# Kernel tuning notes

Measured on AMD Instinct MI355X. Metric: run time of the kernel, lower is better.

Reference implementation:

```python
import jax, jax.numpy as jnp
import numpy as np
import math

NUM_SEGS = 16  # label ids in gt are in [0, NUM_SEGS); 0 = background
NP_RATIO = 3
PI = np.float32(math.pi)


def cart2polar(coord):
    # coord: (N, 2, H, W) -> normalized polar angle in [0, 1)
    x = coord[:, 0]
    y = coord[:, 1]
    theta = jnp.arctan(y / (x + np.float32(1e-12)))
    theta = theta + (x < 0).astype(coord.dtype) * PI
    theta = theta + ((x > 0) & (y < 0)).astype(coord.dtype) * (2 * PI)
    return theta / (2 * PI)


def cal_weight(gt2d):
    # gt2d: (H, W) int labels. Per-segment average weight:
    # each pixel of segment s>0 gets (posCount / nSegPresent) / count(s).
    flat = gt2d.reshape(-1)
    counts = jnp.zeros((NUM_SEGS,), jnp.float32).at[flat].add(1.0)
    pos_counts = counts.at[0].set(0.0)  # labels = unique(gt)[1:] drops background 0
    pos_count = pos_counts.sum()
    nseg = (pos_counts > 0).sum().astype(jnp.float32)
    seg_ave = pos_count / jnp.maximum(nseg, 1.0)
    pix = seg_ave / jnp.maximum(counts, 1.0)  # per-label pixel weight
    return jnp.where(gt2d > 0, pix[gt2d], np.float32(0.0))


def setup_inputs() -> dict:
    key = jax.random.key(0)
    k1, k2, k3 = jax.random.split(key, 3)
    N, C, H, W = 8, 2, 1024, 1024
    pred = jax.random.normal(k1, (N, C, H, W), dtype=jnp.float32)
    gt_df = jax.random.normal(k2, (N, C, H, W), dtype=jnp.float32)
    gt = jax.random.randint(k3, (N, 1, H, W), 0, NUM_SEGS, dtype=jnp.int32)
    return {"pred": pred, "gt_df": gt_df, "gt": gt}


def reference(pred, gt_df, gt):
    N, _, H, W = pred.shape
    dist = pred - gt_df
    distL2 = dist * dist
    angle = cart2polar(gt_df) - cart2polar(pred)          # (N,H,W)
    term = distL2[:, 0] + distL2[:, 1] + angle * angle    # (N,H,W)

    weight = jax.vmap(lambda g: cal_weight(g[0]))(gt)     # (N,H,W) positive-region weights
    regionNeg = (weight == 0).astype(jnp.float32)
    sumPos = (weight > 0).astype(jnp.float32).sum(axis=(1, 2))
    sumNeg = regionNeg.sum(axis=(1, 2))
    k = jnp.minimum(NP_RATIO * sumPos, sumNeg).astype(jnp.int32)  # hard negatives per sample

    # OHEM: keep the k largest negative-region losses per sample
    lossFlat = (term * regionNeg).reshape(N, H * W)
    order = jnp.argsort(lossFlat, axis=1)
    rank = jnp.argsort(order, axis=1)  # rank of each element in ascending order
    keep = rank >= (H * W - k[:, None])
    mask = (keep & (lossFlat != 0)).astype(jnp.float32).reshape(N, H, W)  # weightNeg indicator

    # Faithful to torch broadcast: weightPos (N,H,W) + weightNeg (N,1,H,W) -> (N,N,H,W),
    # computed here without materializing the (N,N,H,W) tensor:
    # sum_{i,j,hw} term[j]*(weight[j] + mask[i]) = N*sum(term*weight) + sum_hw(term.sum(0)*mask.sum(0))
    num = N * jnp.sum(term * weight) + jnp.sum(term.sum(axis=0) * mask.sum(axis=0))
    denom = N * (weight.sum() + mask.sum())
    return num / N / 2.0 / denom
```

## Files before the change

kernel.cpp:

```cpp
#include <hip/hip_runtime.h>
#include <math.h>

#define NBATCH 8
#define HWN (1024*1024)
#define NGRP (HWN/4)
#define MAINB 1024


static __device__ __forceinline__ float polar01(float x, float y) {
    float r = y * __builtin_amdgcn_rcpf(x + 1e-12f);
    float ar = fabsf(r);
    float inv = __builtin_amdgcn_rcpf(ar);
    bool big = ar > 1.0f;
    float t = big ? inv : ar;
    float s = t * t;
    float p = -0.0117212f;
    p = fmaf(p, s,  0.05265332f);
    p = fmaf(p, s, -0.11643287f);
    p = fmaf(p, s,  0.19354346f);
    p = fmaf(p, s, -0.33262348f);
    p = fmaf(p, s,  0.99997726f);
    float a = t * p;
    a = big ? (1.57079632679489662f - a) : a;
    a = copysignf(a, r);
    if (x < 0.f) a += 3.14159274101257324f;
    else if (x > 0.f && y < 0.f) a += 6.28318548202514648f;
    return a * 0.15915494309189535f;
}

static __device__ __forceinline__ void block_reduce2(double& a, double& b) {
    for (int o = 32; o; o >>= 1) { a += __shfl_down(a, o); b += __shfl_down(b, o); }
    __shared__ double sa[4], sb[4];
    int w = threadIdx.x >> 6, l = threadIdx.x & 63;
    if (l == 0) { sa[w] = a; sb[w] = b; }
    __syncthreads();
    if (threadIdx.x == 0) { a = sa[0]+sa[1]+sa[2]+sa[3]; b = sb[0]+sb[1]+sb[2]+sb[3]; }
    __syncthreads();
}

static __device__ __forceinline__ void block_reduce3(double& a, double& b, double& c) {
    for (int o = 32; o; o >>= 1) { a += __shfl_down(a, o); b += __shfl_down(b, o); c += __shfl_down(c, o); }
    __shared__ double sa[4], sb[4], sc[4];
    int w = threadIdx.x >> 6, l = threadIdx.x & 63;
    if (l == 0) { sa[w] = a; sb[w] = b; sc[w] = c; }
    __syncthreads();
    if (threadIdx.x == 0) {
        a = sa[0]+sa[1]+sa[2]+sa[3]; b = sb[0]+sb[1]+sb[2]+sb[3]; c = sc[0]+sc[1]+sc[2]+sc[3];
    }
    __syncthreads();
}

__global__ __launch_bounds__(256) void k_hist(const int* __restrict__ gt,
        unsigned* __restrict__ countsRep) {
    int tid = threadIdx.x;
    int n = blockIdx.x >> 8;
    int jb = blockIdx.x & 255;
    const int4* g4 = (const int4*)(gt + (size_t)n * HWN);
    unsigned c[16];
#pragma unroll
    for (int b = 0; b < 16; ++b) c[b] = 0u;
#pragma unroll
    for (int k = 0; k < 4; ++k) {
        int4 g = g4[jb * 1024 + k * 256 + tid];
#pragma unroll
        for (int e = 0; e < 4; ++e) {
            int gv = (&g.x)[e] & 15;
#pragma unroll
            for (int b = 0; b < 16; ++b) c[b] += (unsigned)__popcll(__ballot(gv == b));
        }
    }
    if ((tid & 63) == 0) {
        int copy = (blockIdx.x * 4 + (tid >> 6)) & 31;
        unsigned* dst = countsRep + copy * 128 + n * 16;
#pragma unroll
        for (int b = 0; b < 16; ++b) atomicAdd(&dst[b], c[b]);
    }
}

__global__ void k_stats(const unsigned* __restrict__ countsRep, float* __restrict__ pix,
                        int* __restrict__ kv, int* __restrict__ mode,
                        double* __restrict__ g_wsum, unsigned* __restrict__ anySlow) {
    int tid = threadIdx.x;
    __shared__ unsigned sc[128];
    __shared__ int smd[NBATCH];
    __shared__ double sws[NBATCH];
    if (tid < 128) {
        unsigned s = 0;
        for (int c = 0; c < 32; ++c) s += countsRep[c * 128 + tid];
        sc[tid] = s;
    }
    __syncthreads();
    if (tid < NBATCH) {
        int n = tid;
        long long sumPos = 0; int nseg = 0;
        for (int s = 1; s < 16; ++s) { sumPos += sc[n*16+s]; nseg += sc[n*16+s] ? 1 : 0; }
        long long sumNeg = sc[n*16];
        float seg_ave = (float)sumPos / (float)(nseg ? nseg : 1);
        double ws = 0.0;
        pix[n*16] = 0.f;
        for (int s = 1; s < 16; ++s) {
            unsigned cc = sc[n*16+s];
            float pv = seg_ave / (float)(cc > 1u ? cc : 1u);
            pix[n*16+s] = pv;
            ws += (double)pv * (double)cc;
        }
        long long k = 3 * sumPos; if (sumNeg < k) k = sumNeg;
        kv[n] = (int)k;
        int md = (k <= 0) ? 0 : ((k >= sumNeg) ? 1 : 2);
        mode[n] = md; smd[n] = md; sws[n] = ws;
    }
    __syncthreads();
    if (tid == 0) {
        double w = 0.0; unsigned as = 0u;
        for (int i = 0; i < NBATCH; ++i) { w += sws[i]; as |= (smd[i] == 2) ? 1u : 0u; }
        *g_wsum = w; *anySlow = as;
    }
}

__global__ __launch_bounds__(256) void k_main(const float* __restrict__ pred,
        const float* __restrict__ gdf, const int* __restrict__ gt,
        const float* __restrict__ pix, const int* __restrict__ mode,
        float* __restrict__ lossBuf, unsigned short* __restrict__ tsumBuf,
        unsigned* __restrict__ h1G, double* __restrict__ pN1,
        double* __restrict__ pS2, double* __restrict__ pC) {
    __shared__ float spix[128];
    __shared__ int smode[NBATCH];
    __shared__ unsigned h1[NBATCH * 256];
    int tid = threadIdx.x;
    if (tid < 128) spix[tid] = pix[tid];
    if (tid < NBATCH) smode[tid] = mode[tid];
    for (int i = tid; i < NBATCH * 256; i += 256) h1[i] = 0u;
    __syncthreads();

    int j = blockIdx.x * 256 + tid;
    float tsum[4] = {0.f, 0.f, 0.f, 0.f};
    int   cntE[4] = {0, 0, 0, 0};
    float num1f = 0.f;
#pragma unroll 2
    for (int n = 0; n < NBATCH; ++n) {
        float4 px4 = ((const float4*)(pred + ((size_t)(2 * n)    ) * HWN))[j];
        float4 py4 = ((const float4*)(pred + ((size_t)(2 * n) + 1) * HWN))[j];
        float4 gx4 = ((const float4*)(gdf  + ((size_t)(2 * n)    ) * HWN))[j];
        float4 gy4 = ((const float4*)(gdf  + ((size_t)(2 * n) + 1) * HWN))[j];
        int4   g4  = ((const int4*)  (gt   + (size_t)n * HWN))[j];
        int m = smode[n];
        float4 lossv;
#pragma unroll
        for (int e = 0; e < 4; ++e) {
            float px = (&px4.x)[e], py = (&py4.x)[e];
            float gx = (&gx4.x)[e], gy = (&gy4.x)[e];
            int   g  = (&g4.x)[e] & 15;
            float dx = px - gx, dy = py - gy;
            float ang = polar01(gx, gy) - polar01(px, py);
            float t = dx * dx + dy * dy + ang * ang;
            tsum[e] += t;
            num1f += t * spix[n * 16 + g];
            if (m == 1) {
                if (g == 0 && t != 0.f) cntE[e]++;
            } else if (m == 2) {
                float lv = (g == 0) ? t : 0.f;
                (&lossv.x)[e] = lv;
                unsigned u = __float_as_uint(lv);
                if (u) atomicAdd(&h1[n * 256 + (u >> 24)], 1u);
            }
        }
        if (m == 2) ((float4*)(lossBuf + (size_t)n * HWN))[j] = lossv;
    }
    ushort4 tz;
#pragma unroll
    for (int e = 0; e < 4; ++e) {
        unsigned u = __float_as_uint(tsum[e]);
        (&tz.x)[e] = (unsigned short)((u + 0x7FFFu + ((u >> 16) & 1u)) >> 16);
    }
    ((ushort4*)tsumBuf)[j] = tz;

    float spec2 = 0.f, cntS = 0.f;
#pragma unroll
    for (int e = 0; e < 4; ++e) { spec2 += tsum[e] * (float)cntE[e]; cntS += (float)cntE[e]; }

    double a = (double)num1f, b = (double)spec2, c = (double)cntS;
    block_reduce3(a, b, c);
    if (tid == 0) { pN1[blockIdx.x] = a; pS2[blockIdx.x] = b; pC[blockIdx.x] = c; }

    __syncthreads();
    int copy = blockIdx.x & 7;
    for (int i = tid; i < NBATCH * 256; i += 256) {
        unsigned v = h1[i];
        if (v) atomicAdd(&h1G[copy * 2048 + i], v);
    }
}

__global__ void k_scanA(const unsigned* __restrict__ h1G, const int* __restrict__ kv,
        const int* __restrict__ mode, unsigned* __restrict__ stMode,
        unsigned* __restrict__ stPfx, unsigned* __restrict__ stK,
        unsigned* __restrict__ stT, unsigned* __restrict__ active,
        const double* __restrict__ pN1, const double* __restrict__ pS2,
        const double* __restrict__ pC, double* __restrict__ g_num1,
        double* __restrict__ g_acc, double* __restrict__ g_cnt) {
    int tid = threadIdx.x;
    double a = 0, b = 0, c = 0;
    for (int i = tid; i < MAINB; i += 256) { a += pN1[i]; b += pS2[i]; c += pC[i]; }
    block_reduce3(a, b, c);
    if (tid == 0) { *g_num1 = a; *g_acc = b; *g_cnt = c; }
    __shared__ unsigned h[256];
    __shared__ unsigned rw[4];
    for (int n = 0; n < NBATCH; ++n) {
        if (mode[n] != 2) continue;
        unsigned s = 0;
        for (int c8 = 0; c8 < 8; ++c8) s += h1G[c8 * 2048 + n * 256 + tid];
        h[tid] = s;
        unsigned v = s;
        for (int o = 32; o; o >>= 1) v += __shfl_down(v, o);
        int w = tid >> 6, l = tid & 63;
        if (l == 0) rw[w] = v;
        __syncthreads();
        if (tid == 0) {
            unsigned nnz = rw[0] + rw[1] + rw[2] + rw[3];
            unsigned k = (unsigned)kv[n];
            if (k >= nnz) { stT[n] = 0u; stMode[n] = 0u; }
            else {
                unsigned cum = 0; int b1 = 0;
                for (int bb = 255; bb >= 0; --bb) { if (cum + h[bb] >= k) { b1 = bb; break; } cum += h[bb]; }
                stMode[n] = 1u; stPfx[n] = (unsigned)b1; stK[n] = k - cum; active[1] = 1u;
            }
        }
        __syncthreads();
    }
}

__global__ __launch_bounds__(256) void k_refine(const float* __restrict__ lossBuf,
        const unsigned* __restrict__ stMode, const unsigned* __restrict__ stPfx,
        unsigned* __restrict__ hist, int level, const unsigned* __restrict__ active) {
    if (active[level] == 0u) return;
    unsigned md[NBATCH], pf[NBATCH];
#pragma unroll
    for (int n = 0; n < NBATCH; ++n) { md[n] = stMode[n]; pf[n] = stPfx[n]; }
    int ms = 32 - 8 * level, hs = 24 - 8 * level;
    int stride = gridDim.x * blockDim.x;
    for (int j = blockIdx.x * blockDim.x + threadIdx.x; j < NGRP; j += stride) {
#pragma unroll
        for (int n = 0; n < NBATCH; ++n) {
            if (md[n] != (unsigned)level) continue;
            float4 lv = ((const float4*)(lossBuf + (size_t)n * HWN))[j];
#pragma unroll
            for (int e = 0; e < 4; ++e) {
                unsigned u = __float_as_uint((&lv.x)[e]);
                if (u != 0u && (u >> ms) == pf[n])
                    atomicAdd(&hist[n * 256 + ((u >> hs) & 255u)], 1u);
            }
        }
    }
}

__global__ void k_scanN(unsigned* __restrict__ stMode, unsigned* __restrict__ stPfx,
        unsigned* __restrict__ stK, unsigned* __restrict__ stT,
        const unsigned* __restrict__ hist, int level, unsigned* __restrict__ active) {
    if (active[level] == 0u) return;
    int n = blockIdx.x;
    if (stMode[n] != (unsigned)level) return;
    __shared__ unsigned h[256];
    h[threadIdx.x] = hist[n * 256 + threadIdx.x];
    __syncthreads();
    if (threadIdx.x == 0) {
        unsigned k2 = stK[n], cum = 0; int bb = 0;
        for (int b = 255; b >= 0; --b) { if (cum + h[b] >= k2) { bb = b; break; } cum += h[b]; }
        unsigned np = (stPfx[n] << 8) | (unsigned)bb;
        stK[n] = k2 - cum;
        if (level == 3) { stT[n] = np; stMode[n] = 0u; }
        else            { stPfx[n] = np; stMode[n] = (unsigned)(level + 1); active[level + 1] = 1u; }
    }
}

__global__ __launch_bounds__(256) void k_num2(const float* __restrict__ lossBuf,
        const unsigned short* __restrict__ tsumBuf, const unsigned* __restrict__ stT,
        const int* __restrict__ mode, const unsigned* __restrict__ anySlow,
        double* __restrict__ g_acc, double* __restrict__ g_cnt) {
    if (*anySlow == 0u) return;
    int j = blockIdx.x * 256 + threadIdx.x;
    ushort4 tz = ((const ushort4*)tsumBuf)[j];
    float ts[4];
#pragma unroll
    for (int e = 0; e < 4; ++e) ts[e] = __uint_as_float(((unsigned)(&tz.x)[e]) << 16);
    double acc = 0.0, cnt = 0.0;
#pragma unroll
    for (int n = 0; n < NBATCH; ++n) {
        if (mode[n] != 2) continue;
        unsigned T = stT[n];
        float4 lv = ((const float4*)(lossBuf + (size_t)n * HWN))[j];
#pragma unroll
        for (int e = 0; e < 4; ++e) {
            unsigned u = __float_as_uint((&lv.x)[e]);
            if (u != 0u && u >= T) { acc += (double)ts[e]; cnt += 1.0; }
        }
    }
    block_reduce2(acc, cnt);
    if (threadIdx.x == 0) { atomicAdd(g_acc, acc); atomicAdd(g_cnt, cnt); }
}

__global__ void k_result(const double* __restrict__ g_num1, const double* __restrict__ g_wsum,
        const double* __restrict__ g_acc, const double* __restrict__ g_cnt,
        float* __restrict__ out) {
    double num = (double)NBATCH * g_num1[0] + g_acc[0];
    double den = (double)NBATCH * (g_wsum[0] + g_cnt[0]);
    out[0] = (float)(num / (double)NBATCH / 2.0 / den);
}


extern "C" void kernel_launch(void* const* d_in, const int* in_sizes, int n_in,
                              void* d_out, int out_size, void* d_ws, size_t ws_size,
                              hipStream_t stream) {
    const float* pred = (const float*)d_in[0];
    const float* gdf  = (const float*)d_in[1];
    const int*   gt   = (const int*)d_in[2];
    float* out = (float*)d_out;

    char* W = (char*)d_ws;
    float* lossBuf = (float*)W;
    unsigned short* tsumBuf = (unsigned short*)(W + 33554432);
    char* Z = W + 35651584;
    unsigned* countsRep = (unsigned*)Z;
    unsigned* h1G    = (unsigned*)(Z + 16384);
    unsigned* hA     = (unsigned*)(Z + 81920);
    unsigned* hB     = (unsigned*)(Z + 90112);
    unsigned* hC     = (unsigned*)(Z + 98304);
    unsigned* stMode = (unsigned*)(Z + 106496);
    unsigned* stPfx  = (unsigned*)(Z + 106528);
    unsigned* stK    = (unsigned*)(Z + 106560);
    unsigned* stT    = (unsigned*)(Z + 106592);
    unsigned* active = (unsigned*)(Z + 106624);
    unsigned* anySlow= (unsigned*)(Z + 106640);
    double*   g_num1 = (double*)(Z + 106648);
    double*   g_wsum = (double*)(Z + 106656);
    double*   g_acc  = (double*)(Z + 106664);
    double*   g_cnt  = (double*)(Z + 106672);
    const size_t ZBYTES = 106680;
    char* P = Z + ZBYTES;
    float* pix  = (float*)P;
    int*   kv   = (int*)(P + 512);
    int*   mode = (int*)(P + 544);
    double* pN1 = (double*)(P + 576);
    double* pS2 = (double*)(P + 8768);
    double* pC  = (double*)(P + 16960);

    size_t need = 35651584 + ZBYTES + 25152;
    if (ws_size < need) return;

    hipMemsetAsync(Z, 0, ZBYTES, stream);
    k_hist  <<<2048, 256, 0, stream>>>(gt, countsRep);
    k_stats <<<1, 256, 0, stream>>>(countsRep, pix, kv, mode, g_wsum, anySlow);
    k_main  <<<MAINB, 256, 0, stream>>>(pred, gdf, gt, pix, mode, lossBuf, tsumBuf,
                                        h1G, pN1, pS2, pC);
    k_scanA <<<1, 256, 0, stream>>>(h1G, kv, mode, stMode, stPfx, stK, stT, active,
                                    pN1, pS2, pC, g_num1, g_acc, g_cnt);
    k_refine<<<1024, 256, 0, stream>>>(lossBuf, stMode, stPfx, hA, 1, active);
    k_scanN <<<NBATCH, 256, 0, stream>>>(stMode, stPfx, stK, stT, hA, 1, active);
    k_refine<<<1024, 256, 0, stream>>>(lossBuf, stMode, stPfx, hB, 2, active);
    k_scanN <<<NBATCH, 256, 0, stream>>>(stMode, stPfx, stK, stT, hB, 2, active);
    k_refine<<<1024, 256, 0, stream>>>(lossBuf, stMode, stPfx, hC, 3, active);
    k_scanN <<<NBATCH, 256, 0, stream>>>(stMode, stPfx, stK, stT, hC, 3, active);
    k_num2  <<<MAINB, 256, 0, stream>>>(lossBuf, tsumBuf, stT, mode, anySlow, g_acc, g_cnt);
    k_result<<<1, 1, 0, stream>>>(g_num1, g_wsum, g_acc, g_cnt, out);
}
```

Measured before the change: 223.1 us.

## Collapse the OHEM pipeline into three kernels with a 16-bit radix histogram

Replaces the memset, stats, scan, three refine, three scan-step, num2 and result launches with three kernels. `k_hist` writes per-block label counts in a transposed layout and zeroes a 64K-bin histogram. `k_main` recomputes per-sample statistics in every block, uses float2 loads, and writes the bf16 tsum buffer only when some sample needs top-k selection. A single-block `k_tail` does the final reductions and a two-level threshold search over the 16-bit histogram. This removes launch and serialization overhead and a 2 MB write in the common case. The price is global atomics on a large histogram and a single-block slow path for the top-k case.

```diff
diff --git a/kernel.cpp b/kernel.cpp
--- a/kernel.cpp
+++ b/kernel.cpp
@@ -3,8 +3,9 @@
 
 #define NBATCH 8
 #define HWN (1024*1024)
-#define NGRP (HWN/4)
-#define MAINB 1024
+#define NPAIR (HWN/2)
+#define HB 512
+#define MB 2048
 
 
 static __device__ __forceinline__ float polar01(float x, float y) {
@@ -40,55 +41,157 @@
 
 static __device__ __forceinline__ void block_reduce3(double& a, double& b, double& c) {
     for (int o = 32; o; o >>= 1) { a += __shfl_down(a, o); b += __shfl_down(b, o); c += __shfl_down(c, o); }
-    __shared__ double sa[4], sb[4], sc[4];
+    __shared__ double sa[4], sb[4], sc4[4];
     int w = threadIdx.x >> 6, l = threadIdx.x & 63;
-    if (l == 0) { sa[w] = a; sb[w] = b; sc[w] = c; }
+    if (l == 0) { sa[w] = a; sb[w] = b; sc4[w] = c; }
     __syncthreads();
     if (threadIdx.x == 0) {
-        a = sa[0]+sa[1]+sa[2]+sa[3]; b = sb[0]+sb[1]+sb[2]+sb[3]; c = sc[0]+sc[1]+sc[2]+sc[3];
-    }
-    __syncthreads();
+        a = sa[0]+sa[1]+sa[2]+sa[3]; b = sb[0]+sb[1]+sb[2]+sb[3]; c = sc4[0]+sc4[1]+sc4[2]+sc4[3];
+    }
+    __syncthreads();
+}
+
+static __device__ __forceinline__ void load_counts(const unsigned* __restrict__ hcntT,
+                                                   unsigned* sc) {
+    int tid = threadIdx.x;
+    if (tid < 128) {
+        int n = tid >> 4, bin = tid & 15;
+        const uint4* p = (const uint4*)&hcntT[bin * HB + n * 64];
+        unsigned s = 0;
+#pragma unroll
+        for (int k = 0; k < 16; ++k) { uint4 v = p[k]; s += v.x + v.y + v.z + v.w; }
+        sc[tid] = s;
+    }
 }
 
 __global__ __launch_bounds__(256) void k_hist(const int* __restrict__ gt,
-        unsigned* __restrict__ countsRep) {
+        unsigned* __restrict__ hcntT, unsigned* __restrict__ h64) {
     int tid = threadIdx.x;
-    int n = blockIdx.x >> 8;
-    int jb = blockIdx.x & 255;
+    uint4 z; z.x = z.y = z.z = z.w = 0u;
+    ((uint4*)h64)[blockIdx.x * 256 + tid] = z;
+
+    int n = blockIdx.x >> 6, b = blockIdx.x & 63;
     const int4* g4 = (const int4*)(gt + (size_t)n * HWN);
     unsigned c[16];
 #pragma unroll
-    for (int b = 0; b < 16; ++b) c[b] = 0u;
-#pragma unroll
-    for (int k = 0; k < 4; ++k) {
-        int4 g = g4[jb * 1024 + k * 256 + tid];
+    for (int bin = 0; bin < 16; ++bin) c[bin] = 0u;
+#pragma unroll
+    for (int k = 0; k < 16; ++k) {
+        int4 g = g4[b * 4096 + k * 256 + tid];
 #pragma unroll
         for (int e = 0; e < 4; ++e) {
             int gv = (&g.x)[e] & 15;
 #pragma unroll
-            for (int b = 0; b < 16; ++b) c[b] += (unsigned)__popcll(__ballot(gv == b));
-        }
-    }
-    if ((tid & 63) == 0) {
-        int copy = (blockIdx.x * 4 + (tid >> 6)) & 31;
-        unsigned* dst = countsRep + copy * 128 + n * 16;
-#pragma unroll
-        for (int b = 0; b < 16; ++b) atomicAdd(&dst[b], c[b]);
-    }
-}
-
-__global__ void k_stats(const unsigned* __restrict__ countsRep, float* __restrict__ pix,
-                        int* __restrict__ kv, int* __restrict__ mode,
-                        double* __restrict__ g_wsum, unsigned* __restrict__ anySlow) {
+            for (int bin = 0; bin < 16; ++bin)
+                c[bin] += (unsigned)__popcll(__ballot(gv == bin));
+        }
+    }
+    __shared__ unsigned sw[4][16];
+    int wave = tid >> 6, lane = tid & 63;
+    if (lane == 0) {
+#pragma unroll
+        for (int bin = 0; bin < 16; ++bin) sw[wave][bin] = c[bin];
+    }
+    __syncthreads();
+    if (tid < 16) hcntT[tid * HB + blockIdx.x] = sw[0][tid] + sw[1][tid] + sw[2][tid] + sw[3][tid];
+}
+
+__global__ __launch_bounds__(256, 8) void k_main(const float* __restrict__ pred,
+        const float* __restrict__ gdf, const int* __restrict__ gt,
+        const unsigned* __restrict__ hcntT, float* __restrict__ lossBuf,
+        unsigned short* __restrict__ tsumBuf, unsigned* __restrict__ h64,
+        double* __restrict__ pN1, double* __restrict__ pS2, double* __restrict__ pC) {
+    __shared__ unsigned sc[128];
+    __shared__ float spix[128];
+    __shared__ int smode[NBATCH];
+    __shared__ int sAny;
     int tid = threadIdx.x;
+    load_counts(hcntT, sc);
+    if (tid == 0) sAny = 0;
+    __syncthreads();
+    if (tid < NBATCH) {
+        int n = tid;
+        long long sumPos = 0; int nseg = 0;
+        for (int s = 1; s < 16; ++s) { sumPos += sc[n*16+s]; nseg += sc[n*16+s] ? 1 : 0; }
+        long long sumNeg = sc[n*16];
+        float seg_ave = (float)sumPos / (float)(nseg ? nseg : 1);
+        spix[n*16] = 0.f;
+        for (int s = 1; s < 16; ++s) {
+            unsigned cc = sc[n*16+s];
+            spix[n*16+s] = seg_ave / (float)(cc > 1u ? cc : 1u);
+        }
+        long long k = 3 * sumPos; if (sumNeg < k) k = sumNeg;
+        int md = (k <= 0) ? 0 : ((k >= sumNeg) ? 1 : 2);
+        smode[n] = md;
+        if (md == 2) sAny = 1;
+    }
+    __syncthreads();
+    bool anySlow = (sAny != 0);
+
+    int j2 = blockIdx.x * 256 + tid;
+    float ts0 = 0.f, ts1 = 0.f, num1f = 0.f;
+    int c0 = 0, c1 = 0;
+#pragma unroll 2
+    for (int n = 0; n < NBATCH; ++n) {
+        float2 px2 = ((const float2*)(pred + ((size_t)(2*n)    ) * HWN))[j2];
+        float2 py2 = ((const float2*)(pred + ((size_t)(2*n) + 1) * HWN))[j2];
+        float2 gx2 = ((const float2*)(gdf  + ((size_t)(2*n)    ) * HWN))[j2];
+        float2 gy2 = ((const float2*)(gdf  + ((size_t)(2*n) + 1) * HWN))[j2];
+        int2   g2  = ((const int2*)  (gt   + (size_t)n * HWN))[j2];
+        int m = smode[n];
+        float dx0 = px2.x - gx2.x, dy0 = py2.x - gy2.x;
+        float a0 = polar01(gx2.x, gy2.x) - polar01(px2.x, py2.x);
+        float t0 = dx0*dx0 + dy0*dy0 + a0*a0;
+        float dx1 = px2.y - gx2.y, dy1 = py2.y - gy2.y;
+        float a1 = polar01(gx2.y, gy2.y) - polar01(px2.y, py2.y);
+        float t1 = dx1*dx1 + dy1*dy1 + a1*a1;
+        int gv0 = g2.x & 15, gv1 = g2.y & 15;
+        ts0 += t0; ts1 += t1;
+        num1f += t0 * spix[n*16 + gv0];
+        num1f += t1 * spix[n*16 + gv1];
+        if (m == 1) {
+            c0 += (gv0 == 0 && t0 != 0.f) ? 1 : 0;
+            c1 += (gv1 == 0 && t1 != 0.f) ? 1 : 0;
+        } else if (m == 2) {
+            float l0 = (gv0 == 0) ? t0 : 0.f;
+            float l1 = (gv1 == 0) ? t1 : 0.f;
+            float2 lv; lv.x = l0; lv.y = l1;
+            ((float2*)(lossBuf + (size_t)n * HWN))[j2] = lv;
+            unsigned u0 = __float_as_uint(l0), u1 = __float_as_uint(l1);
+            unsigned* hh = h64 + (size_t)(blockIdx.x & 7) * 65536;
+            if (u0) atomicAdd(&hh[u0 >> 16], 1u);
+            if (u1) atomicAdd(&hh[u1 >> 16], 1u);
+        }
+    }
+    if (anySlow) {
+        unsigned u0 = __float_as_uint(ts0), u1 = __float_as_uint(ts1);
+        ushort2 tz;
+        tz.x = (unsigned short)((u0 + 0x7FFFu + ((u0 >> 16) & 1u)) >> 16);
+        tz.y = (unsigned short)((u1 + 0x7FFFu + ((u1 >> 16) & 1u)) >> 16);
+        ((ushort2*)tsumBuf)[j2] = tz;
+    }
+    double a = (double)num1f;
+    double b = (double)(ts0 * (float)c0 + ts1 * (float)c1);
+    double c = (double)(c0 + c1);
+    block_reduce3(a, b, c);
+    if (tid == 0) { pN1[blockIdx.x] = a; pS2[blockIdx.x] = b; pC[blockIdx.x] = c; }
+}
+
+__global__ __launch_bounds__(256) void k_tail(const unsigned* __restrict__ hcntT,
+        const unsigned* __restrict__ h64, const float* __restrict__ lossBuf,
+        const unsigned short* __restrict__ tsumBuf, const double* __restrict__ pN1,
+        const double* __restrict__ pS2, const double* __restrict__ pC,
+        float* __restrict__ out) {
     __shared__ unsigned sc[128];
-    __shared__ int smd[NBATCH];
-    __shared__ double sws[NBATCH];
-    if (tid < 128) {
-        unsigned s = 0;
-        for (int c = 0; c < 32; ++c) s += countsRep[c * 128 + tid];
-        sc[tid] = s;
-    }
+    __shared__ double swsum[NBATCH];
+    __shared__ int smode[NBATCH];
+    __shared__ long long skv[NBATCH];
+    __shared__ unsigned part[256];
+    __shared__ unsigned fine[256];
+    __shared__ unsigned scoarse[2];
+    __shared__ double racc[2];
+    int tid = threadIdx.x;
+    load_counts(hcntT, sc);
     __syncthreads();
     if (tid < NBATCH) {
         int n = tid;
@@ -97,212 +200,94 @@
         long long sumNeg = sc[n*16];
         float seg_ave = (float)sumPos / (float)(nseg ? nseg : 1);
         double ws = 0.0;
-        pix[n*16] = 0.f;
         for (int s = 1; s < 16; ++s) {
             unsigned cc = sc[n*16+s];
             float pv = seg_ave / (float)(cc > 1u ? cc : 1u);
-            pix[n*16+s] = pv;
             ws += (double)pv * (double)cc;
         }
         long long k = 3 * sumPos; if (sumNeg < k) k = sumNeg;
-        kv[n] = (int)k;
-        int md = (k <= 0) ? 0 : ((k >= sumNeg) ? 1 : 2);
-        mode[n] = md; smd[n] = md; sws[n] = ws;
-    }
-    __syncthreads();
-    if (tid == 0) {
-        double w = 0.0; unsigned as = 0u;
-        for (int i = 0; i < NBATCH; ++i) { w += sws[i]; as |= (smd[i] == 2) ? 1u : 0u; }
-        *g_wsum = w; *anySlow = as;
-    }
-}
-
-__global__ __launch_bounds__(256) void k_main(const float* __restrict__ pred,
-        const float* __restrict__ gdf, const int* __restrict__ gt,
-        const float* __restrict__ pix, const int* __restrict__ mode,
-        float* __restrict__ lossBuf, unsigned short* __restrict__ tsumBuf,
-        unsigned* __restrict__ h1G, double* __restrict__ pN1,
-        double* __restrict__ pS2, double* __restrict__ pC) {
-    __shared__ float spix[128];
-    __shared__ int smode[NBATCH];
-    __shared__ unsigned h1[NBATCH * 256];
-    int tid = threadIdx.x;
-    if (tid < 128) spix[tid] = pix[tid];
-    if (tid < NBATCH) smode[tid] = mode[tid];
-    for (int i = tid; i < NBATCH * 256; i += 256) h1[i] = 0u;
-    __syncthreads();
-
-    int j = blockIdx.x * 256 + tid;
-    float tsum[4] = {0.f, 0.f, 0.f, 0.f};
-    int   cntE[4] = {0, 0, 0, 0};
-    float num1f = 0.f;
-#pragma unroll 2
+        skv[n] = k;
+        smode[n] = (k <= 0) ? 0 : ((k >= sumNeg) ? 1 : 2);
+        swsum[n] = ws;
+    }
+    __syncthreads();
+
+    double a = 0, b = 0, c = 0;
+    for (int i = tid; i < MB; i += 256) { a += pN1[i]; b += pS2[i]; c += pC[i]; }
+    block_reduce3(a, b, c);
+    if (tid == 0) { racc[0] = b; racc[1] = c; }
+    __syncthreads();
+
     for (int n = 0; n < NBATCH; ++n) {
-        float4 px4 = ((const float4*)(pred + ((size_t)(2 * n)    ) * HWN))[j];
-        float4 py4 = ((const float4*)(pred + ((size_t)(2 * n) + 1) * HWN))[j];
-        float4 gx4 = ((const float4*)(gdf  + ((size_t)(2 * n)    ) * HWN))[j];
-        float4 gy4 = ((const float4*)(gdf  + ((size_t)(2 * n) + 1) * HWN))[j];
-        int4   g4  = ((const int4*)  (gt   + (size_t)n * HWN))[j];
-        int m = smode[n];
-        float4 lossv;
-#pragma unroll
-        for (int e = 0; e < 4; ++e) {
-            float px = (&px4.x)[e], py = (&py4.x)[e];
-            float gx = (&gx4.x)[e], gy = (&gy4.x)[e];
-            int   g  = (&g4.x)[e] & 15;
-            float dx = px - gx, dy = py - gy;
-            float ang = polar01(gx, gy) - polar01(px, py);
-            float t = dx * dx + dy * dy + ang * ang;
-            tsum[e] += t;
-            num1f += t * spix[n * 16 + g];
-            if (m == 1) {
-                if (g == 0 && t != 0.f) cntE[e]++;
-            } else if (m == 2) {
-                float lv = (g == 0) ? t : 0.f;
-                (&lossv.x)[e] = lv;
-                unsigned u = __float_as_uint(lv);
-                if (u) atomicAdd(&h1[n * 256 + (u >> 24)], 1u);
-            }
-        }
-        if (m == 2) ((float4*)(lossBuf + (size_t)n * HWN))[j] = lossv;
-    }
-    ushort4 tz;
-#pragma unroll
-    for (int e = 0; e < 4; ++e) {
-        unsigned u = __float_as_uint(tsum[e]);
-        (&tz.x)[e] = (unsigned short)((u + 0x7FFFu + ((u >> 16) & 1u)) >> 16);
-    }
-    ((ushort4*)tsumBuf)[j] = tz;
-
-    float spec2 = 0.f, cntS = 0.f;
-#pragma unroll
-    for (int e = 0; e < 4; ++e) { spec2 += tsum[e] * (float)cntE[e]; cntS += (float)cntE[e]; }
-
-    double a = (double)num1f, b = (double)spec2, c = (double)cntS;
-    block_reduce3(a, b, c);
-    if (tid == 0) { pN1[blockIdx.x] = a; pS2[blockIdx.x] = b; pC[blockIdx.x] = c; }
-
-    __syncthreads();
-    int copy = blockIdx.x & 7;
-    for (int i = tid; i < NBATCH * 256; i += 256) {
-        unsigned v = h1[i];
-        if (v) atomicAdd(&h1G[copy * 2048 + i], v);
-    }
-}
-
-__global__ void k_scanA(const unsigned* __restrict__ h1G, const int* __restrict__ kv,
-        const int* __restrict__ mode, unsigned* __restrict__ stMode,
-        unsigned* __restrict__ stPfx, unsigned* __restrict__ stK,
-        unsigned* __restrict__ stT, unsigned* __restrict__ active,
-        const double* __restrict__ pN1, const double* __restrict__ pS2,
-        const double* __restrict__ pC, double* __restrict__ g_num1,
-        double* __restrict__ g_acc, double* __restrict__ g_cnt) {
-    int tid = threadIdx.x;
-    double a = 0, b = 0, c = 0;
-    for (int i = tid; i < MAINB; i += 256) { a += pN1[i]; b += pS2[i]; c += pC[i]; }
-    block_reduce3(a, b, c);
-    if (tid == 0) { *g_num1 = a; *g_acc = b; *g_cnt = c; }
-    __shared__ unsigned h[256];
-    __shared__ unsigned rw[4];
-    for (int n = 0; n < NBATCH; ++n) {
-        if (mode[n] != 2) continue;
-        unsigned s = 0;
-        for (int c8 = 0; c8 < 8; ++c8) s += h1G[c8 * 2048 + n * 256 + tid];
-        h[tid] = s;
-        unsigned v = s;
-        for (int o = 32; o; o >>= 1) v += __shfl_down(v, o);
-        int w = tid >> 6, l = tid & 63;
-        if (l == 0) rw[w] = v;
+        if (smode[n] != 2) continue;
+        unsigned loc = 0;
+        int base = tid * 256;
+        for (int i = 0; i < 256; ++i) {
+            unsigned s = 0;
+#pragma unroll
+            for (int r = 0; r < 8; ++r) s += h64[r * 65536 + base + i];
+            loc += s;
+        }
+        part[tid] = loc;
         __syncthreads();
         if (tid == 0) {
-            unsigned nnz = rw[0] + rw[1] + rw[2] + rw[3];
-            unsigned k = (unsigned)kv[n];
-            if (k >= nnz) { stT[n] = 0u; stMode[n] = 0u; }
+            long long nnz = 0;
+            for (int i = 0; i < 256; ++i) nnz += part[i];
+            long long k = skv[n];
+            if (k >= nnz) { scoarse[0] = 0xFFFFFFFFu; }
             else {
-                unsigned cum = 0; int b1 = 0;
-                for (int bb = 255; bb >= 0; --bb) { if (cum + h[bb] >= k) { b1 = bb; break; } cum += h[bb]; }
-                stMode[n] = 1u; stPfx[n] = (unsigned)b1; stK[n] = k - cum; active[1] = 1u;
+                unsigned cum = 0; int cc2 = 0;
+                for (int i = 255; i >= 0; --i) {
+                    if ((long long)cum + part[i] >= k) { cc2 = i; break; }
+                    cum += part[i];
+                }
+                scoarse[0] = (unsigned)cc2; scoarse[1] = cum;
             }
         }
         __syncthreads();
-    }
-}
-
-__global__ __launch_bounds__(256) void k_refine(const float* __restrict__ lossBuf,
-        const unsigned* __restrict__ stMode, const unsigned* __restrict__ stPfx,
-        unsigned* __restrict__ hist, int level, const unsigned* __restrict__ active) {
-    if (active[level] == 0u) return;
-    unsigned md[NBATCH], pf[NBATCH];
-#pragma unroll
-    for (int n = 0; n < NBATCH; ++n) { md[n] = stMode[n]; pf[n] = stPfx[n]; }
-    int ms = 32 - 8 * level, hs = 24 - 8 * level;
-    int stride = gridDim.x * blockDim.x;
-    for (int j = blockIdx.x * blockDim.x + threadIdx.x; j < NGRP; j += stride) {
-#pragma unroll
-        for (int n = 0; n < NBATCH; ++n) {
-            if (md[n] != (unsigned)level) continue;
-            float4 lv = ((const float4*)(lossBuf + (size_t)n * HWN))[j];
-#pragma unroll
-            for (int e = 0; e < 4; ++e) {
-                unsigned u = __float_as_uint((&lv.x)[e]);
-                if (u != 0u && (u >> ms) == pf[n])
-                    atomicAdd(&hist[n * 256 + ((u >> hs) & 255u)], 1u);
+        unsigned T = 0u;
+        if (scoarse[0] != 0xFFFFFFFFu) {
+            unsigned cc2 = scoarse[0];
+            unsigned s = 0;
+#pragma unroll
+            for (int r = 0; r < 8; ++r) s += h64[r * 65536 + cc2 * 256 + tid];
+            fine[tid] = s;
+            __syncthreads();
+            if (tid == 0) {
+                long long k = skv[n];
+                unsigned cum = scoarse[1]; int bb = 0;
+                for (int i = 255; i >= 0; --i) {
+                    if ((long long)cum + fine[i] >= k) { bb = i; break; }
+                    cum += fine[i];
+                }
+                scoarse[0] = (scoarse[0] << 8) | (unsigned)bb;
             }
-        }
-    }
-}
-
-__global__ void k_scanN(unsigned* __restrict__ stMode, unsigned* __restrict__ stPfx,
-        unsigned* __restrict__ stK, unsigned* __restrict__ stT,
-        const unsigned* __restrict__ hist, int level, unsigned* __restrict__ active) {
-    if (active[level] == 0u) return;
-    int n = blockIdx.x;
-    if (stMode[n] != (unsigned)level) return;
-    __shared__ unsigned h[256];
-    h[threadIdx.x] = hist[n * 256 + threadIdx.x];
-    __syncthreads();
-    if (threadIdx.x == 0) {
-        unsigned k2 = stK[n], cum = 0; int bb = 0;
-        for (int b = 255; b >= 0; --b) { if (cum + h[b] >= k2) { bb = b; break; } cum += h[b]; }
-        unsigned np = (stPfx[n] << 8) | (unsigned)bb;
-        stK[n] = k2 - cum;
-        if (level == 3) { stT[n] = np; stMode[n] = 0u; }
-        else            { stPfx[n] = np; stMode[n] = (unsigned)(level + 1); active[level + 1] = 1u; }
-    }
-}
-
-__global__ __launch_bounds__(256) void k_num2(const float* __restrict__ lossBuf,
-        const unsigned short* __restrict__ tsumBuf, const unsigned* __restrict__ stT,
-        const int* __restrict__ mode, const unsigned* __restrict__ anySlow,
-        double* __restrict__ g_acc, double* __restrict__ g_cnt) {
-    if (*anySlow == 0u) return;
-    int j = blockIdx.x * 256 + threadIdx.x;
-    ushort4 tz = ((const ushort4*)tsumBuf)[j];
-    float ts[4];
-#pragma unroll
-    for (int e = 0; e < 4; ++e) ts[e] = __uint_as_float(((unsigned)(&tz.x)[e]) << 16);
-    double acc = 0.0, cnt = 0.0;
-#pragma unroll
-    for (int n = 0; n < NBATCH; ++n) {
-        if (mode[n] != 2) continue;
-        unsigned T = stT[n];
-        float4 lv = ((const float4*)(lossBuf + (size_t)n * HWN))[j];
-#pragma unroll
-        for (int e = 0; e < 4; ++e) {
-            unsigned u = __float_as_uint((&lv.x)[e]);
-            if (u != 0u && u >= T) { acc += (double)ts[e]; cnt += 1.0; }
-        }
-    }
-    block_reduce2(acc, cnt);
-    if (threadIdx.x == 0) { atomicAdd(g_acc, acc); atomicAdd(g_cnt, cnt); }
-}
-
-__global__ void k_result(const double* __restrict__ g_num1, const double* __restrict__ g_wsum,
-        const double* __restrict__ g_acc, const double* __restrict__ g_cnt,
-        float* __restrict__ out) {
-    double num = (double)NBATCH * g_num1[0] + g_acc[0];
-    double den = (double)NBATCH * (g_wsum[0] + g_cnt[0]);
-    out[0] = (float)(num / (double)NBATCH / 2.0 / den);
+            __syncthreads();
+            T = scoarse[0] << 16;
+            __syncthreads();
+        }
+        double acc = 0.0, cnt = 0.0;
+        const float2* lp = (const float2*)(lossBuf + (size_t)n * HWN);
+        const ushort2* tp = (const ushort2*)tsumBuf;
+        for (int i = tid; i < NPAIR; i += 256) {
+            float2 lv = lp[i];
+            ushort2 tz = tp[i];
+            unsigned u0 = __float_as_uint(lv.x), u1 = __float_as_uint(lv.y);
+            if (u0 != 0u && u0 >= T) { acc += (double)__uint_as_float(((unsigned)tz.x) << 16); cnt += 1.0; }
+            if (u1 != 0u && u1 >= T) { acc += (double)__uint_as_float(((unsigned)tz.y) << 16); cnt += 1.0; }
+        }
+        block_reduce2(acc, cnt);
+        if (tid == 0) { racc[0] += acc; racc[1] += cnt; }
+        __syncthreads();
+    }
+
+    if (tid == 0) {
+        double wsum = 0.0;
+        for (int n = 0; n < NBATCH; ++n) wsum += swsum[n];
+        double num = (double)NBATCH * a + racc[0];
+        double den = (double)NBATCH * (wsum + racc[1]);
+        out[0] = (float)(num / (double)NBATCH / 2.0 / den);
+    }
 }
 
 
@@ -317,47 +302,16 @@
     char* W = (char*)d_ws;
     float* lossBuf = (float*)W;
     unsigned short* tsumBuf = (unsigned short*)(W + 33554432);
-    char* Z = W + 35651584;
-    unsigned* countsRep = (unsigned*)Z;
-    unsigned* h1G    = (unsigned*)(Z + 16384);
-    unsigned* hA     = (unsigned*)(Z + 81920);
-    unsigned* hB     = (unsigned*)(Z + 90112);
-    unsigned* hC     = (unsigned*)(Z + 98304);
-    unsigned* stMode = (unsigned*)(Z + 106496);
-    unsigned* stPfx  = (unsigned*)(Z + 106528);
-    unsigned* stK    = (unsigned*)(Z + 106560);
-    unsigned* stT    = (unsigned*)(Z + 106592);
-    unsigned* active = (unsigned*)(Z + 106624);
-    unsigned* anySlow= (unsigned*)(Z + 106640);
-    double*   g_num1 = (double*)(Z + 106648);
-    double*   g_wsum = (double*)(Z + 106656);
-    double*   g_acc  = (double*)(Z + 106664);
-    double*   g_cnt  = (double*)(Z + 106672);
-    const size_t ZBYTES = 106680;
-    char* P = Z + ZBYTES;
-    float* pix  = (float*)P;
-    int*   kv   = (int*)(P + 512);
-    int*   mode = (int*)(P + 544);
-    double* pN1 = (double*)(P + 576);
-    double* pS2 = (double*)(P + 8768);
-    double* pC  = (double*)(P + 16960);
-
-    size_t need = 35651584 + ZBYTES + 25152;
+    unsigned* h64   = (unsigned*)(W + 35651584);
+    unsigned* hcntT = (unsigned*)(W + 37748736);
+    double*   pN1   = (double*)(W + 37781504);
+    double*   pS2   = pN1 + MB;
+    double*   pC    = pS2 + MB;
+
+    size_t need = 37781504 + (size_t)3 * MB * 8;
     if (ws_size < need) return;
 
-    hipMemsetAsync(Z, 0, ZBYTES, stream);
-    k_hist  <<<2048, 256, 0, stream>>>(gt, countsRep);
-    k_stats <<<1, 256, 0, stream>>>(countsRep, pix, kv, mode, g_wsum, anySlow);
-    k_main  <<<MAINB, 256, 0, stream>>>(pred, gdf, gt, pix, mode, lossBuf, tsumBuf,
-                                        h1G, pN1, pS2, pC);
-    k_scanA <<<1, 256, 0, stream>>>(h1G, kv, mode, stMode, stPfx, stK, stT, active,
-                                    pN1, pS2, pC, g_num1, g_acc, g_cnt);
-    k_refine<<<1024, 256, 0, stream>>>(lossBuf, stMode, stPfx, hA, 1, active);
-    k_scanN <<<NBATCH, 256, 0, stream>>>(stMode, stPfx, stK, stT, hA, 1, active);
-    k_refine<<<1024, 256, 0, stream>>>(lossBuf, stMode, stPfx, hB, 2, active);
-    k_scanN <<<NBATCH, 256, 0, stream>>>(stMode, stPfx, stK, stT, hB, 2, active);
-    k_refine<<<1024, 256, 0, stream>>>(lossBuf, stMode, stPfx, hC, 3, active);
-    k_scanN <<<NBATCH, 256, 0, stream>>>(stMode, stPfx, stK, stT, hC, 3, active);
-    k_num2  <<<MAINB, 256, 0, stream>>>(lossBuf, tsumBuf, stT, mode, anySlow, g_acc, g_cnt);
-    k_result<<<1, 1, 0, stream>>>(g_num1, g_wsum, g_acc, g_cnt, out);
-}
+    k_hist<<<HB, 256, 0, stream>>>(gt, hcntT, h64);
+    k_main<<<MB, 256, 0, stream>>>(pred, gdf, gt, hcntT, lossBuf, tsumBuf, h64, pN1, pS2, pC);
+    k_tail<<<1, 256, 0, stream>>>(hcntT, h64, lossBuf, tsumBuf, pN1, pS2, pC, out);
+}
```

Result: no change. 221.3 us (-0.8%).
